# Performance work log

Hardware: AMD Instinct MI355X
Metric: run time of the kernel (lower is better)

## Reference

```python
import jax, jax.numpy as jnp
import numpy as np

LATENT = 64
NUM_FACTORS = 10
INPUT_DIM = 128
BATCH = 64
SEQ = 4096


def setup_inputs() -> dict:
    key = jax.random.key(0)
    ks = jax.random.split(key, 16)
    s = lambda *shape: 1.0 / np.sqrt(shape[-2] if len(shape) > 1 else shape[0])
    inp = {
        "x": jax.random.normal(ks[0], (BATCH, SEQ, INPUT_DIM), dtype=jnp.float32),
        # Conv stack: kernel_size=3, SAME padding, features=LATENT (flax WIO layout)
        "conv_w0": jax.random.normal(ks[1], (3, INPUT_DIM, LATENT), dtype=jnp.float32) * 0.05,
        "conv_b0": jnp.zeros((LATENT,), dtype=jnp.float32),
        "conv_w1": jax.random.normal(ks[2], (3, LATENT, LATENT), dtype=jnp.float32) * 0.05,
        "conv_b1": jnp.zeros((LATENT,), dtype=jnp.float32),
        "conv_w2": jax.random.normal(ks[3], (3, LATENT, LATENT), dtype=jnp.float32) * 0.05,
        "conv_b2": jnp.zeros((LATENT,), dtype=jnp.float32),
        # LSTM layer 0: combined input/hidden projections to 4*LATENT gates (i,f,g,o)
        "Wx0": jax.random.normal(ks[4], (LATENT, 4 * LATENT), dtype=jnp.float32) * 0.05,
        "Wh0": jax.random.normal(ks[5], (LATENT, 4 * LATENT), dtype=jnp.float32) * 0.05,
        "b0": jnp.zeros((4 * LATENT,), dtype=jnp.float32),
        # LSTM layer 1
        "Wx1": jax.random.normal(ks[6], (LATENT, 4 * LATENT), dtype=jnp.float32) * 0.05,
        "Wh1": jax.random.normal(ks[7], (LATENT, 4 * LATENT), dtype=jnp.float32) * 0.05,
        "b1": jnp.zeros((4 * LATENT,), dtype=jnp.float32),
        # Dense head
        "dense_w": jax.random.normal(ks[8], (LATENT, NUM_FACTORS), dtype=jnp.float32) * 0.05,
        "dense_b": jnp.zeros((NUM_FACTORS,), dtype=jnp.float32),
    }
    return inp


def _conv1d_same(x, w, b):
    # x: [B, S, Cin], w: [K, Cin, Cout] (flax WIO); SAME padding, stride 1
    y = jax.lax.conv_general_dilated(
        x, w, window_strides=(1,), padding="SAME",
        dimension_numbers=("NWC", "WIO", "NWC"))
    return y + b


def _lstm_layer(x, Wx, Wh, b):
    # x: [B, S, D] -> returns ((c_final, h_final), outputs [B, S, F])
    B = x.shape[0]
    F = Wh.shape[0]
    xW = jnp.einsum("bsd,dg->bsg", x, Wx)  # precompute input projections [B,S,4F]

    def step(carry, xw_t):
        c, h = carry
        gates = xw_t + h @ Wh + b  # [B, 4F]
        i, f, g, o = jnp.split(gates, 4, axis=-1)
        i = jax.nn.sigmoid(i)
        f = jax.nn.sigmoid(f)
        g = jnp.tanh(g)
        o = jax.nn.sigmoid(o)
        c_new = f * c + i * g
        h_new = o * jnp.tanh(c_new)
        return (c_new, h_new), h_new

    init = (jnp.zeros((B, F), x.dtype), jnp.zeros((B, F), x.dtype))
    (c_f, h_f), ys = jax.lax.scan(step, init, jnp.swapaxes(xW, 0, 1))
    return (c_f, h_f), jnp.swapaxes(ys, 0, 1)


def reference(x, conv_w0, conv_b0, conv_w1, conv_b1, conv_w2, conv_b2,
              Wx0, Wh0, b0, Wx1, Wh1, b1, dense_w, dense_b):
    # CNN stack (eval mode: dropout is identity)
    h = jax.nn.relu(_conv1d_same(x, conv_w0, conv_b0))
    h = jax.nn.relu(_conv1d_same(h, conv_w1, conv_b1))
    h = jax.nn.relu(_conv1d_same(h, conv_w2, conv_b2))
    # Stacked LSTM; keep carry of the LAST layer
    carry, h = _lstm_layer(h, Wx0, Wh0, b0)
    carry, h = _lstm_layer(h, Wx1, Wh1, b1)
    # Original code: final_hidden = carry[0], i.e. the CELL state c (flax carry = (c, h))
    final_hidden = carry[0]  # [B, LATENT]
    latent_factors = final_hidden @ dense_w + dense_b  # [B, NUM_FACTORS]
    return latent_factors
```

## Files before the change

### kernel.cpp

```cpp
#include <hip/hip_runtime.h>
#include <hip/hip_bf16.h>
#include <stdint.h>

#define BATCH 64
#define SEQ   4096
#define CIN   128
#define F     64
#define GATES 256
#define NF    10
#define NSLOT 16

#define CV_OFF    0ull
#define RING_OFF  67108864ull
#define FLAGS_OFF 71303168ull

static __device__ __forceinline__ float sigm(float x) {
  return 1.0f / (1.0f + __expf(-x));
}
static __device__ __forceinline__ float tanh_f(float x) {
  float e = __expf(2.0f * x);
  return 1.0f - 2.0f / (e + 1.0f);
}

template<int NIN, int NROWS, bool TOG>
static __device__ __forceinline__ void conv_stage(
    const float* in, const float* __restrict__ w, const float* __restrict__ bias,
    float* out, float* gout, int gbase, int tbase)
{
  const int tid = threadIdx.x;
  const int cb = (tid & 15) << 2;
  const int pg = tid >> 4;
  constexpr int M = (NROWS + 15) / 16;
  float acc[M][4];
#pragma unroll
  for (int m = 0; m < M; ++m) { acc[m][0] = acc[m][1] = acc[m][2] = acc[m][3] = 0.f; }
#pragma unroll 1
  for (int cc = 0; cc < NIN; cc += 8) {
    float wr[3][8][4];
#pragma unroll
    for (int k = 0; k < 3; ++k)
#pragma unroll
      for (int ci = 0; ci < 8; ++ci) {
        const float4 t = *(const float4*)&w[(k * NIN + cc + ci) * F + cb];
        wr[k][ci][0] = t.x; wr[k][ci][1] = t.y; wr[k][ci][2] = t.z; wr[k][ci][3] = t.w;
      }
#pragma unroll
    for (int m = 0; m < M; ++m) {
      const int r = pg + 16 * m;
      if ((M * 16 == NROWS) || (r < NROWS)) {
#pragma unroll
        for (int k = 0; k < 3; ++k) {
          const float* row = &in[(r + k) * NIN + cc];
          const float4 a  = *(const float4*)&row[0];
          const float4 b4 = *(const float4*)&row[4];
          const float xv[8] = {a.x, a.y, a.z, a.w, b4.x, b4.y, b4.z, b4.w};
#pragma unroll
          for (int ci = 0; ci < 8; ++ci) {
            acc[m][0] += xv[ci] * wr[k][ci][0];
            acc[m][1] += xv[ci] * wr[k][ci][1];
            acc[m][2] += xv[ci] * wr[k][ci][2];
            acc[m][3] += xv[ci] * wr[k][ci][3];
          }
        }
      }
    }
  }
  const float4 bv = *(const float4*)&bias[cb];
#pragma unroll
  for (int m = 0; m < M; ++m) {
    const int r = pg + 16 * m;
    if ((M * 16 == NROWS) || (r < NROWS)) {
      const bool ok = (unsigned)(tbase + r) < (unsigned)SEQ;
      const float o0 = ok ? fmaxf(acc[m][0] + bv.x, 0.f) : 0.f;
      const float o1 = ok ? fmaxf(acc[m][1] + bv.y, 0.f) : 0.f;
      const float o2 = ok ? fmaxf(acc[m][2] + bv.z, 0.f) : 0.f;
      const float o3 = ok ? fmaxf(acc[m][3] + bv.w, 0.f) : 0.f;
      if (TOG) {
        *(float4*)&gout[gbase + r * F + cb] = make_float4(o0, o1, o2, o3);
      } else {
        *(float4*)&out[r * F + cb] = make_float4(o0, o1, o2, o3);
      }
    }
  }
}

__global__ __launch_bounds__(256, 2) void conv_fused(
    const float* __restrict__ x,
    const float* __restrict__ w0, const float* __restrict__ b0,
    const float* __restrict__ w1, const float* __restrict__ b1,
    const float* __restrict__ w2, const float* __restrict__ b2,
    float* __restrict__ cv)
{
  __shared__ __align__(16) float xs[70][CIN];
  __shared__ __align__(16) float y0s[68][F];
  __shared__ __align__(16) float y1s[66][F];
  const int wg  = blockIdx.x;
  const int b   = wg >> 6;
  const int t0  = (wg & 63) << 6;
  const int tid = threadIdx.x;

  const float* xb = x + (size_t)b * SEQ * CIN;
  for (int i = tid; i < 70 * (CIN / 4); i += 256) {
    const int r  = i >> 5;
    const int c4 = (i & 31) << 2;
    const int t  = t0 - 3 + r;
    float4 v = make_float4(0.f, 0.f, 0.f, 0.f);
    if ((unsigned)t < (unsigned)SEQ) v = *(const float4*)&xb[(size_t)t * CIN + c4];
    *(float4*)&xs[r][c4] = v;
  }
  __syncthreads();
  conv_stage<CIN, 68, false>(&xs[0][0], w0, b0, &y0s[0][0], nullptr, 0, t0 - 2);
  __syncthreads();
  conv_stage<F, 66, false>(&y0s[0][0], w1, b1, &y1s[0][0], nullptr, 0, t0 - 1);
  __syncthreads();
  conv_stage<F, 64, true>(&y1s[0][0], w2, b2, nullptr, cv, (b * SEQ + t0) * F, t0);
}

__global__ __launch_bounds__(256, 1) void lstm_scan(
    const float* __restrict__ cv,
    float* __restrict__ ring, uint32_t* __restrict__ flags,
    const float* __restrict__ Wx0, const float* __restrict__ Wh0, const float* __restrict__ bl0,
    const float* __restrict__ Wx1, const float* __restrict__ Wh1, const float* __restrict__ bl1,
    const float* __restrict__ dw, const float* __restrict__ db,
    float* __restrict__ out)
{
  const int  wg   = blockIdx.x;
  const bool prod = (wg < BATCH);
  const int  b    = prod ? wg : (wg - BATCH);
  const int  tid  = threadIdx.x;
  const int  q    = tid & 63;
  const int  kc   = tid >> 6;

  __shared__ __align__(16) float xch[16][F];
  __shared__ __align__(16) float hl[F];
  __shared__ __align__(16) float parts[4][4][F];
  __shared__ __align__(16) float csave[F];

  const float* Wx = prod ? Wx0 : Wx1;
  const float* Wh = prod ? Wh0 : Wh1;
  const float* bb = prod ? bl0 : bl1;

  float wx[4][16], wh[4][16];
#pragma unroll
  for (int g = 0; g < 4; ++g)
#pragma unroll
    for (int kk = 0; kk < 16; ++kk) {
      const int k = (kc << 4) + kk;
      const int j = q + (g << 6);
      wx[g][kk] = Wx[k * GATES + j];
      wh[g][kk] = Wh[k * GATES + j];
    }
  float bias4[4] = {0.f, 0.f, 0.f, 0.f};
  if (tid < F) {
#pragma unroll
    for (int g = 0; g < 4; ++g) bias4[g] = bb[q + (g << 6)];
    hl[tid] = 0.f;
  }
  float creg = 0.f;
  __syncthreads();

  const float* xsrc = cv + (size_t)b * SEQ * F;
  float* myring = ring + (size_t)b * NSLOT * 16 * F;
  uint32_t* prodflag = flags + b * 32;
  uint32_t* consflag = flags + 2048 + b * 32;

#pragma unroll 1
  for (int c = 0; c < SEQ / 16; ++c) {
    const int slot = c & (NSLOT - 1);
    if (prod) {
      const float4 v = *(const float4*)&xsrc[c * 1024 + (tid << 2)];
      ((float4*)&xch[0][0])[tid] = v;
      if (tid == 0) {
        while ((uint32_t)c >= NSLOT + __hip_atomic_load(consflag, __ATOMIC_ACQUIRE, __HIP_MEMORY_SCOPE_AGENT))
          __builtin_amdgcn_s_sleep(2);
      }
      __syncthreads();
    } else {
      while (__hip_atomic_load(prodflag, __ATOMIC_ACQUIRE, __HIP_MEMORY_SCOPE_AGENT) <= (uint32_t)c)
        __builtin_amdgcn_s_sleep(2);
      const float* src = myring + slot * 1024 + (tid << 2);
      float4 f4;
      f4.x = __hip_atomic_load(src + 0, __ATOMIC_RELAXED, __HIP_MEMORY_SCOPE_AGENT);
      f4.y = __hip_atomic_load(src + 1, __ATOMIC_RELAXED, __HIP_MEMORY_SCOPE_AGENT);
      f4.z = __hip_atomic_load(src + 2, __ATOMIC_RELAXED, __HIP_MEMORY_SCOPE_AGENT);
      f4.w = __hip_atomic_load(src + 3, __ATOMIC_RELAXED, __HIP_MEMORY_SCOPE_AGENT);
      ((float4*)&xch[0][0])[tid] = f4;
      __syncthreads();
      if (tid == 0)
        __hip_atomic_store(consflag, (uint32_t)(c + 1),
                           __ATOMIC_RELEASE, __HIP_MEMORY_SCOPE_AGENT);
    }
#pragma unroll 1
    for (int it = 0; it < 16; ++it) {
      float xv[16], hv[16];
      const float4* xp = (const float4*)&xch[it][kc << 4];
      const float4* hp = (const float4*)&hl[kc << 4];
#pragma unroll
      for (int u = 0; u < 4; ++u) {
        const float4 a = xp[u];
        xv[4*u] = a.x; xv[4*u+1] = a.y; xv[4*u+2] = a.z; xv[4*u+3] = a.w;
        const float4 h4 = hp[u];
        hv[4*u] = h4.x; hv[4*u+1] = h4.y; hv[4*u+2] = h4.z; hv[4*u+3] = h4.w;
      }
      float a0 = 0.f, a1 = 0.f, a2 = 0.f, a3 = 0.f;
#pragma unroll
      for (int kk = 0; kk < 16; ++kk) {
        a0 += xv[kk] * wx[0][kk]; a1 += xv[kk] * wx[1][kk];
        a2 += xv[kk] * wx[2][kk]; a3 += xv[kk] * wx[3][kk];
        a0 += hv[kk] * wh[0][kk]; a1 += hv[kk] * wh[1][kk];
        a2 += hv[kk] * wh[2][kk]; a3 += hv[kk] * wh[3][kk];
      }
      parts[kc][0][q] = a0; parts[kc][1][q] = a1;
      parts[kc][2][q] = a2; parts[kc][3][q] = a3;
      __syncthreads();
      if (tid < F) {
        const float s0 = parts[0][0][q] + parts[1][0][q] + parts[2][0][q] + parts[3][0][q] + bias4[0];
        const float s1 = parts[0][1][q] + parts[1][1][q] + parts[2][1][q] + parts[3][1][q] + bias4[1];
        const float s2 = parts[0][2][q] + parts[1][2][q] + parts[2][2][q] + parts[3][2][q] + bias4[2];
        const float s3 = parts[0][3][q] + parts[1][3][q] + parts[2][3][q] + parts[3][3][q] + bias4[3];
        const float iv = sigm(s0);
        const float fv = sigm(s1);
        const float gv = tanh_f(s2);
        const float ov = sigm(s3);
        creg = fv * creg + iv * gv;
        const float hnew = ov * tanh_f(creg);
        hl[q] = hnew;
        if (prod)
          __hip_atomic_store(&myring[slot * 1024 + it * F + q], hnew,
                             __ATOMIC_RELAXED, __HIP_MEMORY_SCOPE_AGENT);
      }
      __syncthreads();
    }
    if (prod && tid == 0)
      __hip_atomic_store(prodflag, (uint32_t)(c + 1),
                         __ATOMIC_RELEASE, __HIP_MEMORY_SCOPE_AGENT);
  }

  if (!prod) {
    if (tid < F) csave[q] = creg;
    __syncthreads();
    if (tid < NF) {
      float acc = db[tid];
#pragma unroll 1
      for (int f = 0; f < F; ++f) acc += csave[f] * dw[f * NF + tid];
      out[b * NF + tid] = acc;
    }
  }
}

extern "C" void kernel_launch(void* const* d_in, const int* in_sizes, int n_in,
                              void* d_out, int out_size, void* d_ws, size_t ws_size,
                              hipStream_t stream) {
  const float* x   = (const float*)d_in[0];
  const float* w0  = (const float*)d_in[1];
  const float* b0  = (const float*)d_in[2];
  const float* w1  = (const float*)d_in[3];
  const float* b1  = (const float*)d_in[4];
  const float* w2  = (const float*)d_in[5];
  const float* b2  = (const float*)d_in[6];
  const float* Wx0 = (const float*)d_in[7];
  const float* Wh0 = (const float*)d_in[8];
  const float* bl0 = (const float*)d_in[9];
  const float* Wx1 = (const float*)d_in[10];
  const float* Wh1 = (const float*)d_in[11];
  const float* bl1 = (const float*)d_in[12];
  const float* dw  = (const float*)d_in[13];
  const float* db  = (const float*)d_in[14];
  float* out = (float*)d_out;

  char* ws = (char*)d_ws;
  float*    cv    = (float*)(ws + CV_OFF);
  float*    ring  = (float*)(ws + RING_OFF);
  uint32_t* flags = (uint32_t*)(ws + FLAGS_OFF);

  hipMemsetAsync(flags, 0, 16384, stream);
  conv_fused<<<dim3(4096), dim3(256), 0, stream>>>(x, w0, b0, w1, b1, w2, b2, cv);
  lstm_scan<<<dim3(128), dim3(256), 0, stream>>>(cv, ring, flags,
                                                 Wx0, Wh0, bl0, Wx1, Wh1, bl1,
                                                 dw, db, out);
}
```

Before: 3.574 ms.

## Fuse both LSTM layers into one workgroup with skewed wavefront schedule

```diff
diff --git a/kernel.cpp b/kernel.cpp
--- a/kernel.cpp
+++ b/kernel.cpp
@@ -8,11 +8,11 @@
 #define F     64
 #define GATES 256
 #define NF    10
-#define NSLOT 16
-
-#define CV_OFF    0ull
-#define RING_OFF  67108864ull
-#define FLAGS_OFF 71303168ull
+#define NCHUNK (SEQ / 16)
+
+#define CV_OFF 0ull
+
+typedef float f32x2 __attribute__((ext_vector_type(2)));
 
 static __device__ __forceinline__ float sigm(float x) {
   return 1.0f / (1.0f + __expf(-x));
@@ -22,7 +22,7 @@
   return 1.0f - 2.0f / (e + 1.0f);
 }
 
-template<int NIN, int NROWS, bool TOG>
+template<int NIN, int LDI, int LDO, int NROWS, bool TOG>
 static __device__ __forceinline__ void conv_stage(
     const float* in, const float* __restrict__ w, const float* __restrict__ bias,
     float* out, float* gout, int gbase, int tbase)
@@ -50,7 +50,7 @@
       if ((M * 16 == NROWS) || (r < NROWS)) {
 #pragma unroll
         for (int k = 0; k < 3; ++k) {
-          const float* row = &in[(r + k) * NIN + cc];
+          const float* row = &in[(r + k) * LDI + cc];
           const float4 a  = *(const float4*)&row[0];
           const float4 b4 = *(const float4*)&row[4];
           const float xv[8] = {a.x, a.y, a.z, a.w, b4.x, b4.y, b4.z, b4.w};
@@ -78,7 +78,7 @@
       if (TOG) {
         *(float4*)&gout[gbase + r * F + cb] = make_float4(o0, o1, o2, o3);
       } else {
-        *(float4*)&out[r * F + cb] = make_float4(o0, o1, o2, o3);
+        *(float4*)&out[r * LDO + cb] = make_float4(o0, o1, o2, o3);
       }
     }
   }
@@ -91,9 +91,9 @@
     const float* __restrict__ w2, const float* __restrict__ b2,
     float* __restrict__ cv)
 {
-  __shared__ __align__(16) float xs[70][CIN];
-  __shared__ __align__(16) float y0s[68][F];
-  __shared__ __align__(16) float y1s[66][F];
+  __shared__ __align__(16) float xs[70 * 132];
+  __shared__ __align__(16) float y0s[68 * 68];
+  __shared__ __align__(16) float y1s[66 * 68];
   const int wg  = blockIdx.x;
   const int b   = wg >> 6;
   const int t0  = (wg & 63) << 6;
@@ -106,145 +106,203 @@
     const int t  = t0 - 3 + r;
     float4 v = make_float4(0.f, 0.f, 0.f, 0.f);
     if ((unsigned)t < (unsigned)SEQ) v = *(const float4*)&xb[(size_t)t * CIN + c4];
-    *(float4*)&xs[r][c4] = v;
+    *(float4*)&xs[r * 132 + c4] = v;
   }
   __syncthreads();
-  conv_stage<CIN, 68, false>(&xs[0][0], w0, b0, &y0s[0][0], nullptr, 0, t0 - 2);
+  conv_stage<CIN, 132, 68, 68, false>(xs, w0, b0, y0s, nullptr, 0, t0 - 2);
   __syncthreads();
-  conv_stage<F, 66, false>(&y0s[0][0], w1, b1, &y1s[0][0], nullptr, 0, t0 - 1);
+  conv_stage<F, 68, 68, 66, false>(y0s, w1, b1, y1s, nullptr, 0, t0 - 1);
   __syncthreads();
-  conv_stage<F, 64, true>(&y1s[0][0], w2, b2, nullptr, cv, (b * SEQ + t0) * F, t0);
-}
-
-__global__ __launch_bounds__(256, 1) void lstm_scan(
+  conv_stage<F, 68, 64, 64, true>(y1s, w2, b2, nullptr, cv, (b * SEQ + t0) * F, t0);
+}
+
+__global__ __launch_bounds__(512, 1) void lstm_scan(
     const float* __restrict__ cv,
-    float* __restrict__ ring, uint32_t* __restrict__ flags,
     const float* __restrict__ Wx0, const float* __restrict__ Wh0, const float* __restrict__ bl0,
     const float* __restrict__ Wx1, const float* __restrict__ Wh1, const float* __restrict__ bl1,
     const float* __restrict__ dw, const float* __restrict__ db,
     float* __restrict__ out)
 {
-  const int  wg   = blockIdx.x;
-  const bool prod = (wg < BATCH);
-  const int  b    = prod ? wg : (wg - BATCH);
-  const int  tid  = threadIdx.x;
-  const int  q    = tid & 63;
-  const int  kc   = tid >> 6;
+  const int b   = blockIdx.x;
+  const int tid = threadIdx.x;
+  const int q   = tid & 63;
+  const int w   = tid >> 6;
+  const int kc  = w & 3;
+  const bool lay0 = (__builtin_amdgcn_readfirstlane(w) < 4);
 
   __shared__ __align__(16) float xch[16][F];
-  __shared__ __align__(16) float hl[F];
-  __shared__ __align__(16) float parts[4][4][F];
+  __shared__ __align__(16) float hh[F];
+  __shared__ __align__(16) float hl1[F];
+  __shared__ __align__(16) f32x2 parts2[8][2][F];
   __shared__ __align__(16) float csave[F];
 
-  const float* Wx = prod ? Wx0 : Wx1;
-  const float* Wh = prod ? Wh0 : Wh1;
-  const float* bb = prod ? bl0 : bl1;
-
-  float wx[4][16], wh[4][16];
+  const float* Wx = lay0 ? Wx0 : Wx1;
+  const float* Wh = lay0 ? Wh0 : Wh1;
+  const float* bb = lay0 ? bl0 : bl1;
+
+  f32x2 wx2[4][8], wh2[4][8];
 #pragma unroll
   for (int g = 0; g < 4; ++g)
 #pragma unroll
-    for (int kk = 0; kk < 16; ++kk) {
-      const int k = (kc << 4) + kk;
+    for (int p = 0; p < 8; ++p) {
+      const int k = (kc << 4) + (p << 1);
       const int j = q + (g << 6);
-      wx[g][kk] = Wx[k * GATES + j];
-      wh[g][kk] = Wh[k * GATES + j];
-    }
-  float bias4[4] = {0.f, 0.f, 0.f, 0.f};
-  if (tid < F) {
-#pragma unroll
-    for (int g = 0; g < 4; ++g) bias4[g] = bb[q + (g << 6)];
-    hl[tid] = 0.f;
-  }
+      wx2[g][p] = f32x2{Wx[k * GATES + j], Wx[(k + 1) * GATES + j]};
+      wh2[g][p] = f32x2{Wh[k * GATES + j], Wh[(k + 1) * GATES + j]};
+    }
+  float biasv[4];
+#pragma unroll
+  for (int g = 0; g < 4; ++g) biasv[g] = (kc == 0) ? bb[q + (g << 6)] : 0.f;
+  if (tid < F) { hh[tid] = 0.f; hl1[tid] = 0.f; }
   float creg = 0.f;
   __syncthreads();
 
   const float* xsrc = cv + (size_t)b * SEQ * F;
-  float* myring = ring + (size_t)b * NSLOT * 16 * F;
-  uint32_t* prodflag = flags + b * 32;
-  uint32_t* consflag = flags + 2048 + b * 32;
+  float4 xreg;
+  if (tid < 256) xreg = *(const float4*)&xsrc[tid << 2];
 
 #pragma unroll 1
-  for (int c = 0; c < SEQ / 16; ++c) {
-    const int slot = c & (NSLOT - 1);
-    if (prod) {
-      const float4 v = *(const float4*)&xsrc[c * 1024 + (tid << 2)];
-      ((float4*)&xch[0][0])[tid] = v;
-      if (tid == 0) {
-        while ((uint32_t)c >= NSLOT + __hip_atomic_load(consflag, __ATOMIC_ACQUIRE, __HIP_MEMORY_SCOPE_AGENT))
-          __builtin_amdgcn_s_sleep(2);
-      }
-      __syncthreads();
-    } else {
-      while (__hip_atomic_load(prodflag, __ATOMIC_ACQUIRE, __HIP_MEMORY_SCOPE_AGENT) <= (uint32_t)c)
-        __builtin_amdgcn_s_sleep(2);
-      const float* src = myring + slot * 1024 + (tid << 2);
-      float4 f4;
-      f4.x = __hip_atomic_load(src + 0, __ATOMIC_RELAXED, __HIP_MEMORY_SCOPE_AGENT);
-      f4.y = __hip_atomic_load(src + 1, __ATOMIC_RELAXED, __HIP_MEMORY_SCOPE_AGENT);
-      f4.z = __hip_atomic_load(src + 2, __ATOMIC_RELAXED, __HIP_MEMORY_SCOPE_AGENT);
-      f4.w = __hip_atomic_load(src + 3, __ATOMIC_RELAXED, __HIP_MEMORY_SCOPE_AGENT);
-      ((float4*)&xch[0][0])[tid] = f4;
-      __syncthreads();
-      if (tid == 0)
-        __hip_atomic_store(consflag, (uint32_t)(c + 1),
-                           __ATOMIC_RELEASE, __HIP_MEMORY_SCOPE_AGENT);
-    }
+  for (int c = 0; c < NCHUNK; ++c) {
+    if (tid < 256) {
+      ((float4*)&xch[0][0])[tid] = xreg;
+      if (c + 1 < NCHUNK)
+        xreg = *(const float4*)&xsrc[(c + 1) * 1024 + (tid << 2)];
+    }
+    __syncthreads();
+
+    f32x2 xv2[8];
+    if (lay0) {
+      const float4* xp4 = (const float4*)&xch[0][kc << 4];
+#pragma unroll
+      for (int u = 0; u < 4; ++u) {
+        const float4 a = xp4[u];
+        xv2[2 * u]     = f32x2{a.x, a.y};
+        xv2[2 * u + 1] = f32x2{a.z, a.w};
+      }
+    }
+
 #pragma unroll 1
     for (int it = 0; it < 16; ++it) {
-      float xv[16], hv[16];
-      const float4* xp = (const float4*)&xch[it][kc << 4];
-      const float4* hp = (const float4*)&hl[kc << 4];
+      f32x2 acc2[4];
+#pragma unroll
+      for (int g = 0; g < 4; ++g) acc2[g] = f32x2{biasv[g], 0.f};
+
+      float4 h0r[4];
+      {
+        const float4* hp4 = (const float4*)&hh[kc << 4];
+#pragma unroll
+        for (int u = 0; u < 4; ++u) h0r[u] = hp4[u];
+      }
+      f32x2 pv[8], qv[8];
+      if (lay0) {
+#pragma unroll
+        for (int p = 0; p < 8; ++p) pv[p] = xv2[p];
+#pragma unroll
+        for (int u = 0; u < 4; ++u) {
+          qv[2 * u]     = f32x2{h0r[u].x, h0r[u].y};
+          qv[2 * u + 1] = f32x2{h0r[u].z, h0r[u].w};
+        }
+      } else {
+        float4 h1r[4];
+        const float4* gp4 = (const float4*)&hl1[kc << 4];
+#pragma unroll
+        for (int u = 0; u < 4; ++u) h1r[u] = gp4[u];
+#pragma unroll
+        for (int u = 0; u < 4; ++u) {
+          pv[2 * u]     = f32x2{h0r[u].x, h0r[u].y};
+          pv[2 * u + 1] = f32x2{h0r[u].z, h0r[u].w};
+          qv[2 * u]     = f32x2{h1r[u].x, h1r[u].y};
+          qv[2 * u + 1] = f32x2{h1r[u].z, h1r[u].w};
+        }
+      }
+#pragma unroll
+      for (int p = 0; p < 8; ++p) {
+        acc2[0] += pv[p] * wx2[0][p]; acc2[1] += pv[p] * wx2[1][p];
+        acc2[2] += pv[p] * wx2[2][p]; acc2[3] += pv[p] * wx2[3][p];
+      }
+#pragma unroll
+      for (int p = 0; p < 8; ++p) {
+        acc2[0] += qv[p] * wh2[0][p]; acc2[1] += qv[p] * wh2[1][p];
+        acc2[2] += qv[p] * wh2[2][p]; acc2[3] += qv[p] * wh2[3][p];
+      }
+      parts2[w][0][q] = f32x2{acc2[0].x + acc2[0].y, acc2[1].x + acc2[1].y};
+      parts2[w][1][q] = f32x2{acc2[2].x + acc2[2].y, acc2[3].x + acc2[3].y};
+      if (lay0 && it < 15) {
+        const float4* xp4 = (const float4*)&xch[it + 1][kc << 4];
+#pragma unroll
+        for (int u = 0; u < 4; ++u) {
+          const float4 a = xp4[u];
+          xv2[2 * u]     = f32x2{a.x, a.y};
+          xv2[2 * u + 1] = f32x2{a.z, a.w};
+        }
+      }
+      __syncthreads();
+      if (kc == 0) {
+        const bool active = lay0 | ((c | it) != 0);
+        if (active) {
+          const f32x2 s01 = parts2[w][0][q] + parts2[w + 1][0][q] + parts2[w + 2][0][q] + parts2[w + 3][0][q];
+          const f32x2 s23 = parts2[w][1][q] + parts2[w + 1][1][q] + parts2[w + 2][1][q] + parts2[w + 3][1][q];
+          const float iv = sigm(s01.x);
+          const float fv = sigm(s01.y);
+          const float gv = tanh_f(s23.x);
+          const float ov = sigm(s23.y);
+          creg = fv * creg + iv * gv;
+          const float hnew = ov * tanh_f(creg);
+          if (lay0) hh[q] = hnew; else hl1[q] = hnew;
+        }
+      }
+      __syncthreads();
+    }
+  }
+
+  {
+    if (!lay0) {
+      f32x2 acc2[4];
+#pragma unroll
+      for (int g = 0; g < 4; ++g) acc2[g] = f32x2{biasv[g], 0.f};
+      float4 h0r[4], h1r[4];
+      {
+        const float4* hp4 = (const float4*)&hh[kc << 4];
+        const float4* gp4 = (const float4*)&hl1[kc << 4];
+#pragma unroll
+        for (int u = 0; u < 4; ++u) { h0r[u] = hp4[u]; h1r[u] = gp4[u]; }
+      }
+      f32x2 pv[8], qv[8];
 #pragma unroll
       for (int u = 0; u < 4; ++u) {
-        const float4 a = xp[u];
-        xv[4*u] = a.x; xv[4*u+1] = a.y; xv[4*u+2] = a.z; xv[4*u+3] = a.w;
-        const float4 h4 = hp[u];
-        hv[4*u] = h4.x; hv[4*u+1] = h4.y; hv[4*u+2] = h4.z; hv[4*u+3] = h4.w;
-      }
-      float a0 = 0.f, a1 = 0.f, a2 = 0.f, a3 = 0.f;
-#pragma unroll
-      for (int kk = 0; kk < 16; ++kk) {
-        a0 += xv[kk] * wx[0][kk]; a1 += xv[kk] * wx[1][kk];
-        a2 += xv[kk] * wx[2][kk]; a3 += xv[kk] * wx[3][kk];
-        a0 += hv[kk] * wh[0][kk]; a1 += hv[kk] * wh[1][kk];
-        a2 += hv[kk] * wh[2][kk]; a3 += hv[kk] * wh[3][kk];
-      }
-      parts[kc][0][q] = a0; parts[kc][1][q] = a1;
-      parts[kc][2][q] = a2; parts[kc][3][q] = a3;
-      __syncthreads();
-      if (tid < F) {
-        const float s0 = parts[0][0][q] + parts[1][0][q] + parts[2][0][q] + parts[3][0][q] + bias4[0];
-        const float s1 = parts[0][1][q] + parts[1][1][q] + parts[2][1][q] + parts[3][1][q] + bias4[1];
-        const float s2 = parts[0][2][q] + parts[1][2][q] + parts[2][2][q] + parts[3][2][q] + bias4[2];
-        const float s3 = parts[0][3][q] + parts[1][3][q] + parts[2][3][q] + parts[3][3][q] + bias4[3];
-        const float iv = sigm(s0);
-        const float fv = sigm(s1);
-        const float gv = tanh_f(s2);
-        const float ov = sigm(s3);
-        creg = fv * creg + iv * gv;
-        const float hnew = ov * tanh_f(creg);
-        hl[q] = hnew;
-        if (prod)
-          __hip_atomic_store(&myring[slot * 1024 + it * F + q], hnew,
-                             __ATOMIC_RELAXED, __HIP_MEMORY_SCOPE_AGENT);
-      }
-      __syncthreads();
-    }
-    if (prod && tid == 0)
-      __hip_atomic_store(prodflag, (uint32_t)(c + 1),
-                         __ATOMIC_RELEASE, __HIP_MEMORY_SCOPE_AGENT);
-  }
-
-  if (!prod) {
-    if (tid < F) csave[q] = creg;
+        pv[2 * u]     = f32x2{h0r[u].x, h0r[u].y};
+        pv[2 * u + 1] = f32x2{h0r[u].z, h0r[u].w};
+        qv[2 * u]     = f32x2{h1r[u].x, h1r[u].y};
+        qv[2 * u + 1] = f32x2{h1r[u].z, h1r[u].w};
+      }
+#pragma unroll
+      for (int p = 0; p < 8; ++p) {
+        acc2[0] += pv[p] * wx2[0][p]; acc2[1] += pv[p] * wx2[1][p];
+        acc2[2] += pv[p] * wx2[2][p]; acc2[3] += pv[p] * wx2[3][p];
+        acc2[0] += qv[p] * wh2[0][p]; acc2[1] += qv[p] * wh2[1][p];
+        acc2[2] += qv[p] * wh2[2][p]; acc2[3] += qv[p] * wh2[3][p];
+      }
+      parts2[w][0][q] = f32x2{acc2[0].x + acc2[0].y, acc2[1].x + acc2[1].y};
+      parts2[w][1][q] = f32x2{acc2[2].x + acc2[2].y, acc2[3].x + acc2[3].y};
+    }
     __syncthreads();
-    if (tid < NF) {
-      float acc = db[tid];
+    if (w == 4) {
+      const f32x2 s01 = parts2[4][0][q] + parts2[5][0][q] + parts2[6][0][q] + parts2[7][0][q];
+      const f32x2 s23 = parts2[4][1][q] + parts2[5][1][q] + parts2[6][1][q] + parts2[7][1][q];
+      const float iv = sigm(s01.x);
+      const float fv = sigm(s01.y);
+      const float gv = tanh_f(s23.x);
+      creg = fv * creg + iv * gv;
+      csave[q] = creg;
+    }
+    __syncthreads();
+  }
+
+  if (tid < NF) {
+    float acc = db[tid];
 #pragma unroll 1
-      for (int f = 0; f < F; ++f) acc += csave[f] * dw[f * NF + tid];
-      out[b * NF + tid] = acc;
-    }
+    for (int f = 0; f < F; ++f) acc += csave[f] * dw[f * NF + tid];
+    out[b * NF + tid] = acc;
   }
 }
 
@@ -268,14 +326,10 @@
   const float* db  = (const float*)d_in[14];
   float* out = (float*)d_out;
 
-  char* ws = (char*)d_ws;
-  float*    cv    = (float*)(ws + CV_OFF);
-  float*    ring  = (float*)(ws + RING_OFF);
-  uint32_t* flags = (uint32_t*)(ws + FLAGS_OFF);
-
-  hipMemsetAsync(flags, 0, 16384, stream);
+  float* cv = (float*)((char*)d_ws + CV_OFF);
+
   conv_fused<<<dim3(4096), dim3(256), 0, stream>>>(x, w0, b0, w1, b1, w2, b2, cv);
-  lstm_scan<<<dim3(128), dim3(256), 0, stream>>>(cv, ring, flags,
-                                                 Wx0, Wh0, bl0, Wx1, Wh1, bl1,
-                                                 dw, db, out);
-}
+  lstm_scan<<<dim3(64), dim3(512), 0, stream>>>(cv,
+                                                Wx0, Wh0, bl0, Wx1, Wh1, bl1,
+                                                dw, db, out);
+}
```

After: 4.297 ms. +20.2%, slower.

## Restructure LSTM scan to per-thread full-dot gates with shuffles and batched ring writes

Applied to the files above, without the earlier changes.

```diff
diff --git a/kernel.cpp b/kernel.cpp
--- a/kernel.cpp
+++ b/kernel.cpp
@@ -9,20 +9,15 @@
 #define GATES 256
 #define NF    10
 #define NSLOT 16
+#define NCHUNK (SEQ / 16)
 
 #define CV_OFF    0ull
 #define RING_OFF  67108864ull
 #define FLAGS_OFF 71303168ull
 
-static __device__ __forceinline__ float sigm(float x) {
-  return 1.0f / (1.0f + __expf(-x));
-}
-static __device__ __forceinline__ float tanh_f(float x) {
-  float e = __expf(2.0f * x);
-  return 1.0f - 2.0f / (e + 1.0f);
-}
-
-template<int NIN, int NROWS, bool TOG>
+typedef float f32x2 __attribute__((ext_vector_type(2)));
+
+template<int NIN, int LDI, int LDO, int NROWS, bool TOG>
 static __device__ __forceinline__ void conv_stage(
     const float* in, const float* __restrict__ w, const float* __restrict__ bias,
     float* out, float* gout, int gbase, int tbase)
@@ -31,18 +26,24 @@
   const int cb = (tid & 15) << 2;
   const int pg = tid >> 4;
   constexpr int M = (NROWS + 15) / 16;
-  float acc[M][4];
-#pragma unroll
-  for (int m = 0; m < M; ++m) { acc[m][0] = acc[m][1] = acc[m][2] = acc[m][3] = 0.f; }
+  f32x2 acc2[M][4];
+#pragma unroll
+  for (int m = 0; m < M; ++m)
+#pragma unroll
+    for (int o = 0; o < 4; ++o) acc2[m][o] = f32x2{0.f, 0.f};
 #pragma unroll 1
   for (int cc = 0; cc < NIN; cc += 8) {
-    float wr[3][8][4];
+    f32x2 wr2[3][4][4];
 #pragma unroll
     for (int k = 0; k < 3; ++k)
 #pragma unroll
-      for (int ci = 0; ci < 8; ++ci) {
-        const float4 t = *(const float4*)&w[(k * NIN + cc + ci) * F + cb];
-        wr[k][ci][0] = t.x; wr[k][ci][1] = t.y; wr[k][ci][2] = t.z; wr[k][ci][3] = t.w;
+      for (int p = 0; p < 4; ++p) {
+        const float4 t0 = *(const float4*)&w[(k * NIN + cc + 2 * p) * F + cb];
+        const float4 t1 = *(const float4*)&w[(k * NIN + cc + 2 * p + 1) * F + cb];
+        wr2[k][p][0] = f32x2{t0.x, t1.x};
+        wr2[k][p][1] = f32x2{t0.y, t1.y};
+        wr2[k][p][2] = f32x2{t0.z, t1.z};
+        wr2[k][p][3] = f32x2{t0.w, t1.w};
       }
 #pragma unroll
     for (int m = 0; m < M; ++m) {
@@ -50,16 +51,15 @@
       if ((M * 16 == NROWS) || (r < NROWS)) {
 #pragma unroll
         for (int k = 0; k < 3; ++k) {
-          const float* row = &in[(r + k) * NIN + cc];
+          const float* row = &in[(r + k) * LDI + cc];
           const float4 a  = *(const float4*)&row[0];
           const float4 b4 = *(const float4*)&row[4];
-          const float xv[8] = {a.x, a.y, a.z, a.w, b4.x, b4.y, b4.z, b4.w};
-#pragma unroll
-          for (int ci = 0; ci < 8; ++ci) {
-            acc[m][0] += xv[ci] * wr[k][ci][0];
-            acc[m][1] += xv[ci] * wr[k][ci][1];
-            acc[m][2] += xv[ci] * wr[k][ci][2];
-            acc[m][3] += xv[ci] * wr[k][ci][3];
+          const f32x2 xp[4] = {{a.x, a.y}, {a.z, a.w}, {b4.x, b4.y}, {b4.z, b4.w}};
+#pragma unroll
+          for (int p = 0; p < 4; ++p) {
+#pragma unroll
+            for (int o = 0; o < 4; ++o)
+              acc2[m][o] += xp[p] * wr2[k][p][o];
           }
         }
       }
@@ -71,14 +71,14 @@
     const int r = pg + 16 * m;
     if ((M * 16 == NROWS) || (r < NROWS)) {
       const bool ok = (unsigned)(tbase + r) < (unsigned)SEQ;
-      const float o0 = ok ? fmaxf(acc[m][0] + bv.x, 0.f) : 0.f;
-      const float o1 = ok ? fmaxf(acc[m][1] + bv.y, 0.f) : 0.f;
-      const float o2 = ok ? fmaxf(acc[m][2] + bv.z, 0.f) : 0.f;
-      const float o3 = ok ? fmaxf(acc[m][3] + bv.w, 0.f) : 0.f;
+      const float o0 = ok ? fmaxf(acc2[m][0].x + acc2[m][0].y + bv.x, 0.f) : 0.f;
+      const float o1 = ok ? fmaxf(acc2[m][1].x + acc2[m][1].y + bv.y, 0.f) : 0.f;
+      const float o2 = ok ? fmaxf(acc2[m][2].x + acc2[m][2].y + bv.z, 0.f) : 0.f;
+      const float o3 = ok ? fmaxf(acc2[m][3].x + acc2[m][3].y + bv.w, 0.f) : 0.f;
       if (TOG) {
         *(float4*)&gout[gbase + r * F + cb] = make_float4(o0, o1, o2, o3);
       } else {
-        *(float4*)&out[r * F + cb] = make_float4(o0, o1, o2, o3);
+        *(float4*)&out[r * LDO + cb] = make_float4(o0, o1, o2, o3);
       }
     }
   }
@@ -91,9 +91,9 @@
     const float* __restrict__ w2, const float* __restrict__ b2,
     float* __restrict__ cv)
 {
-  __shared__ __align__(16) float xs[70][CIN];
-  __shared__ __align__(16) float y0s[68][F];
-  __shared__ __align__(16) float y1s[66][F];
+  __shared__ __align__(16) float xs[70 * 132];
+  __shared__ __align__(16) float y0s[68 * 68];
+  __shared__ __align__(16) float y1s[66 * 68];
   const int wg  = blockIdx.x;
   const int b   = wg >> 6;
   const int t0  = (wg & 63) << 6;
@@ -106,14 +106,14 @@
     const int t  = t0 - 3 + r;
     float4 v = make_float4(0.f, 0.f, 0.f, 0.f);
     if ((unsigned)t < (unsigned)SEQ) v = *(const float4*)&xb[(size_t)t * CIN + c4];
-    *(float4*)&xs[r][c4] = v;
-  }
-  __syncthreads();
-  conv_stage<CIN, 68, false>(&xs[0][0], w0, b0, &y0s[0][0], nullptr, 0, t0 - 2);
-  __syncthreads();
-  conv_stage<F, 66, false>(&y0s[0][0], w1, b1, &y1s[0][0], nullptr, 0, t0 - 1);
-  __syncthreads();
-  conv_stage<F, 64, true>(&y1s[0][0], w2, b2, nullptr, cv, (b * SEQ + t0) * F, t0);
+    *(float4*)&xs[r * 132 + c4] = v;
+  }
+  __syncthreads();
+  conv_stage<CIN, 132, 68, 68, false>(xs, w0, b0, y0s, nullptr, 0, t0 - 2);
+  __syncthreads();
+  conv_stage<F, 68, 68, 66, false>(y0s, w1, b1, y1s, nullptr, 0, t0 - 1);
+  __syncthreads();
+  conv_stage<F, 68, 64, 64, true>(y1s, w2, b2, nullptr, cv, (b * SEQ + t0) * F, t0);
 }
 
 __global__ __launch_bounds__(256, 1) void lstm_scan(
@@ -128,34 +128,30 @@
   const bool prod = (wg < BATCH);
   const int  b    = prod ? wg : (wg - BATCH);
   const int  tid  = threadIdx.x;
-  const int  q    = tid & 63;
-  const int  kc   = tid >> 6;
+  const int  l    = tid & 63;
+  const int  w    = tid >> 6;
+  const int  qi   = l >> 2;
+  const int  gb   = l & 3;
+  const int  q    = (w << 4) + qi;
 
   __shared__ __align__(16) float xch[16][F];
-  __shared__ __align__(16) float hl[F];
-  __shared__ __align__(16) float parts[4][4][F];
+  __shared__ __align__(16) float hl[2][F];
+  __shared__ __align__(16) float hh[16][F];
   __shared__ __align__(16) float csave[F];
 
   const float* Wx = prod ? Wx0 : Wx1;
   const float* Wh = prod ? Wh0 : Wh1;
   const float* bb = prod ? bl0 : bl1;
-
-  float wx[4][16], wh[4][16];
-#pragma unroll
-  for (int g = 0; g < 4; ++g)
-#pragma unroll
-    for (int kk = 0; kk < 16; ++kk) {
-      const int k = (kc << 4) + kk;
-      const int j = q + (g << 6);
-      wx[g][kk] = Wx[k * GATES + j];
-      wh[g][kk] = Wh[k * GATES + j];
-    }
-  float bias4[4] = {0.f, 0.f, 0.f, 0.f};
-  if (tid < F) {
-#pragma unroll
-    for (int g = 0; g < 4; ++g) bias4[g] = bb[q + (g << 6)];
-    hl[tid] = 0.f;
-  }
+  const int j = (gb << 6) + q;
+
+  f32x2 wx2[32], wh2[32];
+#pragma unroll
+  for (int p = 0; p < 32; ++p) {
+    wx2[p] = f32x2{Wx[(2 * p) * GATES + j], Wx[(2 * p + 1) * GATES + j]};
+    wh2[p] = f32x2{Wh[(2 * p) * GATES + j], Wh[(2 * p + 1) * GATES + j]};
+  }
+  const float bias = bb[j];
+  if (tid < F) { hl[0][tid] = 0.f; hl[1][tid] = 0.f; }
   float creg = 0.f;
   __syncthreads();
 
@@ -164,17 +160,16 @@
   uint32_t* prodflag = flags + b * 32;
   uint32_t* consflag = flags + 2048 + b * 32;
 
-#pragma unroll 1
-  for (int c = 0; c < SEQ / 16; ++c) {
+  float4 xreg;
+  if (prod) xreg = *(const float4*)&xsrc[tid << 2];
+
+#pragma unroll 1
+  for (int c = 0; c < NCHUNK; ++c) {
     const int slot = c & (NSLOT - 1);
     if (prod) {
-      const float4 v = *(const float4*)&xsrc[c * 1024 + (tid << 2)];
-      ((float4*)&xch[0][0])[tid] = v;
-      if (tid == 0) {
-        while ((uint32_t)c >= NSLOT + __hip_atomic_load(consflag, __ATOMIC_ACQUIRE, __HIP_MEMORY_SCOPE_AGENT))
-          __builtin_amdgcn_s_sleep(2);
-      }
-      __syncthreads();
+      ((float4*)&xch[0][0])[tid] = xreg;
+      if (c + 1 < NCHUNK)
+        xreg = *(const float4*)&xsrc[(c + 1) * 1024 + (tid << 2)];
     } else {
       while (__hip_atomic_load(prodflag, __ATOMIC_ACQUIRE, __HIP_MEMORY_SCOPE_AGENT) <= (uint32_t)c)
         __builtin_amdgcn_s_sleep(2);
@@ -185,59 +180,79 @@
       f4.z = __hip_atomic_load(src + 2, __ATOMIC_RELAXED, __HIP_MEMORY_SCOPE_AGENT);
       f4.w = __hip_atomic_load(src + 3, __ATOMIC_RELAXED, __HIP_MEMORY_SCOPE_AGENT);
       ((float4*)&xch[0][0])[tid] = f4;
+    }
+    __syncthreads();
+    if (!prod && tid == 0)
+      __hip_atomic_store(consflag, (uint32_t)(c + 1),
+                         __ATOMIC_RELEASE, __HIP_MEMORY_SCOPE_AGENT);
+
+    float4 xcur[16];
+    {
+      const float4* xp = (const float4*)&xch[0][0];
+#pragma unroll
+      for (int m = 0; m < 16; ++m) xcur[m] = xp[m];
+    }
+
+#pragma unroll 1
+    for (int it = 0; it < 16; ++it) {
+      const int rb = it & 1;
+      float4 hq[16];
+      {
+        const float4* hp = (const float4*)&hl[rb][0];
+#pragma unroll
+        for (int m = 0; m < 16; ++m) hq[m] = hp[m];
+      }
+      f32x2 a0{0.f, 0.f}, a1{0.f, 0.f}, a2{0.f, 0.f}, a3{0.f, 0.f};
+#pragma unroll
+      for (int m = 0; m < 16; ++m) {
+        a0 += f32x2{xcur[m].x, xcur[m].y} * wx2[2 * m];
+        a1 += f32x2{xcur[m].z, xcur[m].w} * wx2[2 * m + 1];
+      }
+#pragma unroll
+      for (int m = 0; m < 16; ++m) {
+        a2 += f32x2{hq[m].x, hq[m].y} * wh2[2 * m];
+        a3 += f32x2{hq[m].z, hq[m].w} * wh2[2 * m + 1];
+      }
+      if (it < 15) {
+        const float4* xp = (const float4*)&xch[it + 1][0];
+#pragma unroll
+        for (int m = 0; m < 16; ++m) xcur[m] = xp[m];
+      }
+      const float s = ((a0.x + a0.y) + (a1.x + a1.y)) +
+                      ((a2.x + a2.y) + (a3.x + a3.y)) + bias;
+      const bool isg = (gb == 2);
+      const float aa = isg ? (-2.f * s) : (-s);
+      const float e  = __expf(aa);
+      const float rr = __builtin_amdgcn_rcpf(1.f + e);
+      const float act = isg ? (2.f * rr - 1.f) : rr;
+      const float fv = __shfl_down(act, 1);
+      const float gv = __shfl_down(act, 2);
+      const float ov = __shfl_down(act, 3);
+      if (gb == 0) {
+        creg = fv * creg + act * gv;
+        const float e2 = __expf(-2.f * creg);
+        const float th = 2.f * __builtin_amdgcn_rcpf(1.f + e2) - 1.f;
+        const float hnew = ov * th;
+        hl[rb ^ 1][q] = hnew;
+        hh[it][q] = hnew;
+      }
+      __syncthreads();
+    }
+
+    if (prod) {
+      while ((uint32_t)c >= NSLOT + __hip_atomic_load(consflag, __ATOMIC_ACQUIRE, __HIP_MEMORY_SCOPE_AGENT))
+        __builtin_amdgcn_s_sleep(2);
+      float* dst = myring + slot * 1024;
+      *(float4*)&dst[tid << 2] = ((const float4*)&hh[0][0])[tid];
       __syncthreads();
       if (tid == 0)
-        __hip_atomic_store(consflag, (uint32_t)(c + 1),
+        __hip_atomic_store(prodflag, (uint32_t)(c + 1),
                            __ATOMIC_RELEASE, __HIP_MEMORY_SCOPE_AGENT);
     }
-#pragma unroll 1
-    for (int it = 0; it < 16; ++it) {
-      float xv[16], hv[16];
-      const float4* xp = (const float4*)&xch[it][kc << 4];
-      const float4* hp = (const float4*)&hl[kc << 4];
-#pragma unroll
-      for (int u = 0; u < 4; ++u) {
-        const float4 a = xp[u];
-        xv[4*u] = a.x; xv[4*u+1] = a.y; xv[4*u+2] = a.z; xv[4*u+3] = a.w;
-        const float4 h4 = hp[u];
-        hv[4*u] = h4.x; hv[4*u+1] = h4.y; hv[4*u+2] = h4.z; hv[4*u+3] = h4.w;
-      }
-      float a0 = 0.f, a1 = 0.f, a2 = 0.f, a3 = 0.f;
-#pragma unroll
-      for (int kk = 0; kk < 16; ++kk) {
-        a0 += xv[kk] * wx[0][kk]; a1 += xv[kk] * wx[1][kk];
-        a2 += xv[kk] * wx[2][kk]; a3 += xv[kk] * wx[3][kk];
-        a0 += hv[kk] * wh[0][kk]; a1 += hv[kk] * wh[1][kk];
-        a2 += hv[kk] * wh[2][kk]; a3 += hv[kk] * wh[3][kk];
-      }
-      parts[kc][0][q] = a0; parts[kc][1][q] = a1;
-      parts[kc][2][q] = a2; parts[kc][3][q] = a3;
-      __syncthreads();
-      if (tid < F) {
-        const float s0 = parts[0][0][q] + parts[1][0][q] + parts[2][0][q] + parts[3][0][q] + bias4[0];
-        const float s1 = parts[0][1][q] + parts[1][1][q] + parts[2][1][q] + parts[3][1][q] + bias4[1];
-        const float s2 = parts[0][2][q] + parts[1][2][q] + parts[2][2][q] + parts[3][2][q] + bias4[2];
-        const float s3 = parts[0][3][q] + parts[1][3][q] + parts[2][3][q] + parts[3][3][q] + bias4[3];
-        const float iv = sigm(s0);
-        const float fv = sigm(s1);
-        const float gv = tanh_f(s2);
-        const float ov = sigm(s3);
-        creg = fv * creg + iv * gv;
-        const float hnew = ov * tanh_f(creg);
-        hl[q] = hnew;
-        if (prod)
-          __hip_atomic_store(&myring[slot * 1024 + it * F + q], hnew,
-                             __ATOMIC_RELAXED, __HIP_MEMORY_SCOPE_AGENT);
-      }
-      __syncthreads();
-    }
-    if (prod && tid == 0)
-      __hip_atomic_store(prodflag, (uint32_t)(c + 1),
-                         __ATOMIC_RELEASE, __HIP_MEMORY_SCOPE_AGENT);
   }
 
   if (!prod) {
-    if (tid < F) csave[q] = creg;
+    if (gb == 0) csave[q] = creg;
     __syncthreads();
     if (tid < NF) {
       float acc = db[tid];
```

Result: slower. 4.007 ms (+12.1%).
